# Kernel optimization log

Hardware: AMD Instinct MI355X
Metric: run time of the kernel (lower is better)

Reference implementation:

```python
import jax, jax.numpy as jnp
import numpy as np

BN_EPS = 1e-5

def setup_inputs() -> dict:
    key = jax.random.key(0)
    k1, k2, k3 = jax.random.split(key, 3)
    B, C, H, W = 8, 96, 56, 56
    Cout = 2 * C  # must equal 2*C for the BatchNorm in the original module
    x = jax.random.normal(k1, (B, C, H, W), dtype=jnp.float32)
    conv_w = jax.random.normal(k2, (Cout, 2 * C), dtype=jnp.float32) * (1.0 / np.sqrt(2 * C))
    conv_b = jax.random.normal(k3, (Cout,), dtype=jnp.float32) * 0.01
    gamma = jnp.ones((Cout,), dtype=jnp.float32)
    beta = jnp.zeros((Cout,), dtype=jnp.float32)
    return {"x": x, "conv_w": conv_w, "conv_b": conv_b, "gamma": gamma, "beta": beta}

def _forward(x, conv_w, conv_b, gamma, beta):
    B, C, H, W = x.shape
    # b c h w -> b n c, n = H*W
    q = x.reshape(B, C, H * W).transpose(0, 2, 1)
    # unscaled self-attention (q == k == v == tokens)
    att = jnp.einsum('bnc,bmc->bnm', q, q)          # [B, N, N]
    att = jax.nn.softmax(att, axis=-1)
    att = jnp.einsum('bnm,bmc->bnc', att, q)        # [B, N, C]
    att = att.transpose(0, 2, 1).reshape(B, C, H, W)
    # max-relative: x_j = max(0, x - att) since x_j starts at zeros
    x_j = jnp.maximum(x - att, 0.0)
    cat = jnp.concatenate([x, x_j], axis=1)          # [B, 2C, H, W]
    # 1x1 conv
    y = jnp.einsum('bchw,oc->bohw', cat, conv_w) + conv_b[None, :, None, None]
    # BatchNorm2d in training mode: biased batch stats over (B, H, W)
    mean = jnp.mean(y, axis=(0, 2, 3), keepdims=True)
    var = jnp.var(y, axis=(0, 2, 3), keepdims=True)
    y = (y - mean) * jax.lax.rsqrt(var + BN_EPS)
    y = y * gamma[None, :, None, None] + beta[None, :, None, None]
    # torch nn.GELU default is exact (erf) GELU
    return jax.nn.gelu(y, approximate=False)

def reference(x, conv_w, conv_b, gamma, beta):
    return _forward(x, conv_w, conv_b, gamma, beta)
```

## Files before the change

### kernel.cpp

```cpp
#include <hip/hip_runtime.h>
#include <hip/hip_bf16.h>

#define B_    8
#define C_    96
#define N_    3136
#define COUT_ 192
#define NTOK_ 25088
#define BN_EPS 1e-5f

#define CROW 200
#define BNC  (B_ * N_ * C_)
#define NSPLIT 4
#define NT98  98

#define K2_KL_OFF 7168
#define K2_V_OFF  14336
#define K2_BUFSZ  22528

typedef __hip_bfloat16 bf16;
typedef unsigned short u16;
typedef unsigned int u32;
typedef __attribute__((ext_vector_type(8))) short short8;
typedef __attribute__((ext_vector_type(16))) float f32x16;

__device__ __forceinline__ u16 f2bf(float f) {
    union { __hip_bfloat16 h; u16 u; } cv;
    cv.h = __float2bfloat16(f);
    return cv.u;
}
__device__ __forceinline__ float bf2f(u16 v) {
    union { u16 u; __hip_bfloat16 h; } cv;
    cv.u = v;
    return __bfloat162float(cv.h);
}
__device__ __forceinline__ u32 packbf2(float lo, float hi) {
    return ((u32)f2bf(hi) << 16) | (u32)f2bf(lo);
}

__device__ __forceinline__ void gload_lds16(const void* g, void* l) {
    __builtin_amdgcn_global_load_lds((const __attribute__((address_space(1))) void*)g,
                                     (__attribute__((address_space(3))) void*)l,
                                     16, 0, 0);
}

__global__ __launch_bounds__(256) void transpose_split(const float* __restrict__ x,
                                                       u16* __restrict__ xt_hi,
                                                       u16* __restrict__ xt_lo,
                                                       u16* __restrict__ xc_hi,
                                                       float* __restrict__ norm2) {
    __shared__ float tile[32][33];
    __shared__ float nrm[32];
    const int nb = blockIdx.x * 32;
    const int cb = blockIdx.y * 32;
    const int b  = blockIdx.z;
    const int tid = threadIdx.x;
    const int tx = tid & 31;
    const int ty = tid >> 5;
    if (tid < 32) nrm[tid] = 0.0f;
    float psum = 0.0f;
#pragma unroll
    for (int r = 0; r < 32; r += 8) {
        size_t idx = ((size_t)b * C_ + cb + ty + r) * N_ + nb + tx;
        float v = x[idx];
        tile[ty + r][tx] = v;
        xc_hi[idx] = f2bf(v);
        psum = fmaf(v, v, psum);
    }
    __syncthreads();
    atomicAdd(&nrm[tx], psum);
#pragma unroll
    for (int it = 0; it < 2; it++) {
        const int n2 = (tid >> 4) + it * 16;
        const int cp = tid & 15;
        float v0 = tile[2 * cp][n2];
        float v1 = tile[2 * cp + 1][n2];
        u16 h0 = f2bf(v0), h1 = f2bf(v1);
        u16 l0 = f2bf(v0 - bf2f(h0)), l1 = f2bf(v1 - bf2f(h1));
        size_t o = ((size_t)b * N_ + nb + n2) * C_ + cb + 2 * cp;
        *(u32*)&xt_hi[o] = (u32)h0 | ((u32)h1 << 16);
        *(u32*)&xt_lo[o] = (u32)l0 | ((u32)l1 << 16);
    }
    __syncthreads();
    if (tid < 32)
        atomicAdd(&norm2[(size_t)b * N_ + nb + tid], nrm[tid]);
}

__global__ __launch_bounds__(256) void cast_w(const float* __restrict__ w,
                                              u16* __restrict__ whi,
                                              u16* __restrict__ wlo) {
    int i = blockIdx.x * 256 + threadIdx.x;
    if (i >= COUT_ * 2 * C_) return;
    float v = w[i];
    u16 h = f2bf(v);
    whi[i] = h;
    wlo[i] = f2bf(v - bf2f(h));
}

__global__ __launch_bounds__(256) void norm_max(const float* __restrict__ norm2,
                                                int* __restrict__ maxbits) {
    const int tid = blockIdx.x * 256 + threadIdx.x;
    float m = 0.0f;
    for (int i = tid; i < NTOK_; i += gridDim.x * 256) m = fmaxf(m, norm2[i]);
#pragma unroll
    for (int d = 1; d < 64; d <<= 1) m = fmaxf(m, __shfl_xor(m, d));
    if ((threadIdx.x & 63) == 0) atomicMax(maxbits, __float_as_int(m));
}

__global__ __launch_bounds__(256, 3) void flash_attn_mfma32(const u16* __restrict__ xt_hi,
                                                            const u16* __restrict__ xt_lo,
                                                            const u16* __restrict__ xc_hi,
                                                            const float* __restrict__ norm2,
                                                            const int* __restrict__ maxbits,
                                                            float* __restrict__ attT,
                                                            float* __restrict__ l_arr) {
    __shared__ __align__(16) char LDSU[2][K2_BUFSZ];
    const int b     = blockIdx.y;
    const int i0    = blockIdx.x * 128;
    const int split = blockIdx.z;
    const int kt0   = (NT98 * split) / NSPLIT;
    const int kt1   = (NT98 * (split + 1)) / NSPLIT;
    const int tid   = threadIdx.x;
    const int lane  = tid & 63;
    const int w     = tid >> 6;
    const int col   = lane & 31;
    const int g     = lane >> 5;

    const u16* th = xt_hi + (size_t)b * N_ * C_;
    const u16* tl = xt_lo + (size_t)b * N_ * C_;
    const u16* vh = xc_hi + (size_t)b * C_ * N_;

    u32 loff[6], dofs[6];
#pragma unroll
    for (int j = 0; j < 6; j++) {
        int s = w + 4 * j;
        if (s >= 22) { loff[j] = 0; dofs[j] = 0; continue; }
        if (s < 14) {
            int kind = s < 7 ? 0 : 1;
            int t = s - kind * 7;
            int p = t * 64 + lane;
            int r = p / 13, c = p % 13;
            if (c > 11) c = 11;
            loff[j] = (r < 32) ? (u32)(r * 192 + c * 16) : 0u;
            dofs[j] = (u32)(kind * K2_KL_OFF + t * 1024);
        } else {
            int t = s - 14;
            int p = t * 64 + lane;
            int ch = p / 5, c = p % 5;
            if (c > 3) c = 3;
            loff[j] = (ch < 96) ? (u32)(ch * (N_ * 2) + c * 16) : 0u;
            dofs[j] = (u32)(K2_V_OFF + t * 1024);
        }
    }

    const int qrow  = i0 + w * 32 + col;
    const int qrowc = qrow < N_ ? qrow : N_ - 1;
    short8 qh[6], ql[6];
#pragma unroll
    for (int kc = 0; kc < 6; kc++) {
        qh[kc] = *(const short8*)&th[(size_t)qrowc * C_ + kc * 16 + g * 8];
        ql[kc] = *(const short8*)&tl[(size_t)qrowc * C_ + kc * 16 + g * 8];
    }
    const float maxn2 = __int_as_float(*maxbits);
    const float m_i   = sqrtf(norm2[(size_t)b * N_ + qrowc] * maxn2);
    float l_acc = 0.0f;
    f32x16 O0 = {0}, O1 = {0}, O2 = {0};

    auto stage = [&](int nbuf, int kt) {
        const u32 ktK = (u32)kt * 6144u;
        const u32 ktV = (u32)kt * 64u;
#pragma unroll
        for (int j = 0; j < 6; j++) {
            int s = w + 4 * j;
            if (s >= 22) break;
            const char* sb = (s < 7)  ? (const char*)th + ktK
                           : (s < 14) ? (const char*)tl + ktK
                                      : (const char*)vh + ktV;
            gload_lds16(sb + loff[j], (char*)&LDSU[nbuf][0] + dofs[j]);
        }
    };

    stage(0, kt0);
    __syncthreads();

    const int g16 = g * 16;
    int buf = 0;
    for (int kt = kt0; kt < kt1; kt++) {
        if (kt + 1 < kt1) stage(buf ^ 1, kt + 1);

        const char* Lb = (const char*)&LDSU[buf][0];

        f32x16 S = {0};
        __builtin_amdgcn_s_setprio(1);
#pragma unroll
        for (int kc = 0; kc < 6; kc++) {
            const int o2 = col * 208 + kc * 32 + g16;
            short8 kh = *(const short8*)(Lb + o2);
            short8 kl = *(const short8*)(Lb + K2_KL_OFF + o2);
            S = __builtin_amdgcn_mfma_f32_32x32x16_bf16(kh, ql[kc], S, 0, 0, 0);
            S = __builtin_amdgcn_mfma_f32_32x32x16_bf16(kl, qh[kc], S, 0, 0, 0);
            S = __builtin_amdgcn_mfma_f32_32x32x16_bf16(kh, qh[kc], S, 0, 0, 0);
        }
        __builtin_amdgcn_s_setprio(0);

        float p[16];
#pragma unroll
        for (int r = 0; r < 16; r++) {
            p[r] = __expf(S[r] - m_i);
            l_acc += p[r];
        }
        u32 w8[8];
#pragma unroll
        for (int q = 0; q < 8; q++) w8[q] = packbf2(p[2 * q], p[2 * q + 1]);

        __builtin_amdgcn_s_setprio(1);
#pragma unroll
        for (int kc = 0; kc < 2; kc++) {
            const int qb = kc * 4;
            u32 a0 = w8[qb + 0], a1 = w8[qb + 1];
            u32 a2 = w8[qb + 2], a3 = w8[qb + 3];
            u32 s0 = __shfl_xor((int)a0, 32), s1 = __shfl_xor((int)a1, 32);
            u32 s2 = __shfl_xor((int)a2, 32), s3 = __shfl_xor((int)a3, 32);
            union { short8 v; u32 u[4]; } Bf;
            Bf.u[0] = g ? s2 : a0;
            Bf.u[1] = g ? s3 : a1;
            Bf.u[2] = g ? a2 : s0;
            Bf.u[3] = g ? a3 : s1;
            const int vo = K2_V_OFF + col * 80 + kc * 32 + g16;
            short8 v0 = *(const short8*)(Lb + vo);
            short8 v1 = *(const short8*)(Lb + vo + 2560);
            short8 v2 = *(const short8*)(Lb + vo + 5120);
            O0 = __builtin_amdgcn_mfma_f32_32x32x16_bf16(v0, Bf.v, O0, 0, 0, 0);
            O1 = __builtin_amdgcn_mfma_f32_32x32x16_bf16(v1, Bf.v, O1, 0, 0, 0);
            O2 = __builtin_amdgcn_mfma_f32_32x32x16_bf16(v2, Bf.v, O2, 0, 0, 0);
        }
        __builtin_amdgcn_s_setprio(0);

        __syncthreads();
        buf ^= 1;
    }

    if (qrow < N_) {
        float* ab = attT + (size_t)b * C_ * N_ + qrow;
#pragma unroll
        for (int r = 0; r < 16; r++) {
            int c = (r & 3) + 8 * (r >> 2) + 4 * g;
            atomicAdd(&ab[(size_t)(c)      * N_], O0[r]);
            atomicAdd(&ab[(size_t)(c + 32) * N_], O1[r]);
            atomicAdd(&ab[(size_t)(c + 64) * N_], O2[r]);
        }
        float l_tot = l_acc + __shfl_xor(l_acc, 32);
        if (g == 0) atomicAdd(&l_arr[(size_t)b * N_ + qrow], l_tot);
    }
}

__global__ __launch_bounds__(128, 3) void conv_mfma(const float* __restrict__ x,
                                                    const float* __restrict__ attT,
                                                    const float* __restrict__ l_arr,
                                                    const u16* __restrict__ whi,
                                                    const u16* __restrict__ wlo,
                                                    const float* __restrict__ convb,
                                                    float* __restrict__ y) {
    __shared__ u16 ch[32 * CROW];
    __shared__ u16 cl[32 * CROW];
    __shared__ float invl[32];
    const int b   = blockIdx.x / (N_ / 32);
    const int n0  = (blockIdx.x % (N_ / 32)) * 32;
    const int tid = threadIdx.x;

    if (tid < 32) invl[tid] = 1.0f / l_arr[(size_t)b * N_ + n0 + tid];
    __syncthreads();

    const float* xb = x    + (size_t)b * C_ * N_ + n0;
    const float* ab = attT + (size_t)b * C_ * N_ + n0;
    for (int e = tid; e < 32 * C_; e += 128) {
        int c = e >> 5, t = e & 31;
        float xv = xb[(size_t)c * N_ + t];
        float au = ab[(size_t)c * N_ + t];
        float xj = fmaxf(xv - au * invl[t], 0.0f);
        u16 h1 = f2bf(xv);
        ch[t * CROW + c] = h1;
        cl[t * CROW + c] = f2bf(xv - bf2f(h1));
        u16 h2 = f2bf(xj);
        ch[t * CROW + C_ + c] = h2;
        cl[t * CROW + C_ + c] = f2bf(xj - bf2f(h2));
    }
    __syncthreads();

    const int lane = tid & 63;
    const int w    = tid >> 6;
    const int col  = lane & 31;
    const int g    = lane >> 5;
    const int m0   = w * 3;

    f32x16 A[3] = {{0}, {0}, {0}};
#pragma unroll
    for (int ks = 0; ks < 12; ks++) {
        const int k0 = ks * 16;
        short8 bh = *(const short8*)&ch[col * CROW + k0 + g * 8];
        short8 bl = *(const short8*)&cl[col * CROW + k0 + g * 8];
#pragma unroll
        for (int mt = 0; mt < 3; mt++) {
            const size_t wo = (size_t)((m0 + mt) * 32 + col) * (2 * C_) + k0 + g * 8;
            short8 ah = *(const short8*)&whi[wo];
            short8 al = *(const short8*)&wlo[wo];
            A[mt] = __builtin_amdgcn_mfma_f32_32x32x16_bf16(ah, bl, A[mt], 0, 0, 0);
            A[mt] = __builtin_amdgcn_mfma_f32_32x32x16_bf16(al, bh, A[mt], 0, 0, 0);
            A[mt] = __builtin_amdgcn_mfma_f32_32x32x16_bf16(ah, bh, A[mt], 0, 0, 0);
        }
    }

    float* yb = y + (size_t)b * COUT_ * N_ + n0 + col;
#pragma unroll
    for (int mt = 0; mt < 3; mt++)
#pragma unroll
        for (int r = 0; r < 16; r++) {
            int o = (m0 + mt) * 32 + (r & 3) + 8 * (r >> 2) + 4 * g;
            yb[(size_t)o * N_] = A[mt][r] + convb[o];
        }
}

__global__ __launch_bounds__(256) void bn_partial(const float* __restrict__ y,
                                                  float* __restrict__ pb) {
    const int o   = blockIdx.x;
    const int b   = blockIdx.y;
    const int tid = threadIdx.x;
    float s = 0.0f, q = 0.0f;
    const float4* p = (const float4*)(y + (size_t)(b * COUT_ + o) * N_);
    for (int i = tid; i < N_ / 4; i += 256) {
        float4 v = p[i];
        s += v.x + v.y + v.z + v.w;
        q += v.x * v.x + v.y * v.y + v.z * v.z + v.w * v.w;
    }
#pragma unroll
    for (int d = 1; d < 64; d <<= 1) {
        s += __shfl_xor(s, d);
        q += __shfl_xor(q, d);
    }
    __shared__ float wss[4], wqq[4];
    if ((tid & 63) == 0) { wss[tid >> 6] = s; wqq[tid >> 6] = q; }
    __syncthreads();
    if (tid == 0) {
        pb[b * COUT_ + o]                = wss[0] + wss[1] + wss[2] + wss[3];
        pb[B_ * COUT_ + b * COUT_ + o]   = wqq[0] + wqq[1] + wqq[2] + wqq[3];
    }
}

__global__ __launch_bounds__(192) void bn_finish(const float* __restrict__ pb,
                                                 const float* __restrict__ gamma,
                                                 const float* __restrict__ beta,
                                                 float* __restrict__ ss) {
    const int o = threadIdx.x;
    float s = 0.0f, q = 0.0f;
#pragma unroll
    for (int b = 0; b < B_; b++) {
        s += pb[b * COUT_ + o];
        q += pb[B_ * COUT_ + b * COUT_ + o];
    }
    const float invn = 1.0f / (float)NTOK_;
    float mean = s * invn;
    float var  = q * invn - mean * mean;
    float sc   = gamma[o] * rsqrtf(var + BN_EPS);
    ss[o]         = sc;
    ss[COUT_ + o] = beta[o] - mean * sc;
}

__global__ __launch_bounds__(256) void bn_gelu_out(const float* __restrict__ y,
                                                   const float* __restrict__ ss,
                                                   float* __restrict__ out) {
    const int total4 = (B_ * COUT_ * N_) / 4;
    int i = blockIdx.x * 256 + threadIdx.x;
    if (i >= total4) return;
    int base = i * 4;
    int o = (base / N_) % COUT_;
    float sc = ss[o], sh = ss[COUT_ + o];
    float4 v = *(const float4*)&y[base];
    float u0 = fmaf(v.x, sc, sh), u1 = fmaf(v.y, sc, sh);
    float u2 = fmaf(v.z, sc, sh), u3 = fmaf(v.w, sc, sh);
    const float k = 0.70710678118654752f;
    float4 g;
    g.x = 0.5f * u0 * (1.0f + erff(u0 * k));
    g.y = 0.5f * u1 * (1.0f + erff(u1 * k));
    g.z = 0.5f * u2 * (1.0f + erff(u2 * k));
    g.w = 0.5f * u3 * (1.0f + erff(u3 * k));
    *(float4*)&out[base] = g;
}

extern "C" void kernel_launch(void* const* d_in, const int* in_sizes, int n_in,
                              void* d_out, int out_size, void* d_ws, size_t ws_size,
                              hipStream_t stream) {
    const float* x     = (const float*)d_in[0];
    const float* w     = (const float*)d_in[1];
    const float* cb    = (const float*)d_in[2];
    const float* gamma = (const float*)d_in[3];
    const float* beta  = (const float*)d_in[4];

    u16* xt_hi = (u16*)d_ws;
    u16* xt_lo = xt_hi + (size_t)BNC;
    u16* xc_hi = xt_lo + (size_t)BNC;
    float* attT  = (float*)(xc_hi + (size_t)BNC);
    u16* whi   = (u16*)(attT + (size_t)BNC);
    u16* wlo   = whi + COUT_ * 2 * C_;
    float* y     = (float*)(wlo + COUT_ * 2 * C_);
    float* ss    = y + (size_t)B_ * COUT_ * N_;
    float* l_arr = ss + 2 * COUT_;
    float* norm2 = l_arr + NTOK_;
    int*   maxb  = (int*)(norm2 + NTOK_);
    float* pb    = attT;

    hipMemsetAsync(l_arr, 0, NTOK_ * sizeof(float), stream);
    hipMemsetAsync(norm2, 0, NTOK_ * sizeof(float), stream);
    hipMemsetAsync(maxb, 0, sizeof(int), stream);
    hipMemsetAsync(attT, 0, (size_t)BNC * sizeof(float), stream);

    transpose_split<<<dim3(N_ / 32, C_ / 32, B_), 256, 0, stream>>>(x, xt_hi, xt_lo, xc_hi, norm2);
    cast_w<<<dim3((COUT_ * 2 * C_ + 255) / 256), 256, 0, stream>>>(w, whi, wlo);
    norm_max<<<dim3(25), 256, 0, stream>>>(norm2, maxb);
    flash_attn_mfma32<<<dim3((N_ + 127) / 128, B_, NSPLIT), 256, 0, stream>>>(
        xt_hi, xt_lo, xc_hi, norm2, maxb, attT, l_arr);
    conv_mfma<<<dim3(B_ * (N_ / 32)), 128, 0, stream>>>(x, attT, l_arr, whi, wlo, cb, y);
    bn_partial<<<dim3(COUT_, B_), 256, 0, stream>>>(y, pb);
    bn_finish<<<dim3(1), 192, 0, stream>>>(pb, gamma, beta, ss);
    bn_gelu_out<<<dim3((B_ * COUT_ * N_ / 4 + 255) / 256), 256, 0, stream>>>(y, ss, (float*)d_out);
}
```

Before: 223.7 us.

## Store tokens in MFMA-fragment layout and load K directly from global

The transpose kernel now writes the bf16 hi/lo token matrices in a pre-swizzled layout where each 32-token by 16-channel MFMA operand is a contiguous 512-element block. The attention kernel then loads K fragments straight from global memory (L2-cached) with one 16-byte load per lane, and no longer stages K through LDS. Only V stays double-buffered in LDS. This cuts LDS traffic and footprint, which may allow higher occupancy, but K reads now carry global/L2 latency inside the inner loop with only light software pipelining.

```diff
diff --git a/kernel.cpp b/kernel.cpp
--- a/kernel.cpp
+++ b/kernel.cpp
@@ -13,10 +13,6 @@
 #define NSPLIT 4
 #define NT98  98
 
-#define K2_KL_OFF 7168
-#define K2_V_OFF  14336
-#define K2_BUFSZ  22528
-
 typedef __hip_bfloat16 bf16;
 typedef unsigned short u16;
 typedef unsigned int u32;
@@ -43,9 +39,13 @@
                                      16, 0, 0);
 }
 
+__device__ __forceinline__ size_t foff(int t, int kc) {
+    return ((size_t)t * 6 + kc) << 9;
+}
+
 __global__ __launch_bounds__(256) void transpose_split(const float* __restrict__ x,
-                                                       u16* __restrict__ xt_hi,
-                                                       u16* __restrict__ xt_lo,
+                                                       u16* __restrict__ xf_hi,
+                                                       u16* __restrict__ xf_lo,
                                                        u16* __restrict__ xc_hi,
                                                        float* __restrict__ norm2) {
     __shared__ float tile[32][33];
@@ -68,17 +68,23 @@
     }
     __syncthreads();
     atomicAdd(&nrm[tx], psum);
-#pragma unroll
-    for (int it = 0; it < 2; it++) {
-        const int n2 = (tid >> 4) + it * 16;
-        const int cp = tid & 15;
-        float v0 = tile[2 * cp][n2];
-        float v1 = tile[2 * cp + 1][n2];
-        u16 h0 = f2bf(v0), h1 = f2bf(v1);
-        u16 l0 = f2bf(v0 - bf2f(h0)), l1 = f2bf(v1 - bf2f(h1));
-        size_t o = ((size_t)b * N_ + nb + n2) * C_ + cb + 2 * cp;
-        *(u32*)&xt_hi[o] = (u32)h0 | ((u32)h1 << 16);
-        *(u32*)&xt_lo[o] = (u32)l0 | ((u32)l1 << 16);
+
+    {
+        const int item  = tid & 127;
+        const int is_lo = tid >> 7;
+        const int kc_i  = item >> 6;
+        const int l     = item & 63;
+        const int kcg   = (cb >> 4) + kc_i;
+        union { u16 a[8]; short8 v8; } o;
+#pragma unroll
+        for (int j = 0; j < 8; j++) {
+            float v = tile[kc_i * 16 + ((l >> 5) * 8) + j][l & 31];
+            u16 h = f2bf(v);
+            o.a[j] = is_lo ? f2bf(v - bf2f(h)) : h;
+        }
+        u16* dst = (is_lo ? xf_lo : xf_hi) +
+                   ((size_t)b * NT98 * 6 << 9) + foff(nb >> 5, kcg) + l * 8;
+        *(short8*)dst = o.v8;
     }
     __syncthreads();
     if (tid < 32)
@@ -106,14 +112,14 @@
     if ((threadIdx.x & 63) == 0) atomicMax(maxbits, __float_as_int(m));
 }
 
-__global__ __launch_bounds__(256, 3) void flash_attn_mfma32(const u16* __restrict__ xt_hi,
-                                                            const u16* __restrict__ xt_lo,
+__global__ __launch_bounds__(256, 3) void flash_attn_mfma32(const u16* __restrict__ xf_hi,
+                                                            const u16* __restrict__ xf_lo,
                                                             const u16* __restrict__ xc_hi,
                                                             const float* __restrict__ norm2,
                                                             const int* __restrict__ maxbits,
                                                             float* __restrict__ attT,
                                                             float* __restrict__ l_arr) {
-    __shared__ __align__(16) char LDSU[2][K2_BUFSZ];
+    __shared__ __align__(16) char VL[2][8192];
     const int b     = blockIdx.y;
     const int i0    = blockIdx.x * 128;
     const int split = blockIdx.z;
@@ -125,82 +131,70 @@
     const int col   = lane & 31;
     const int g     = lane >> 5;
 
-    const u16* th = xt_hi + (size_t)b * N_ * C_;
-    const u16* tl = xt_lo + (size_t)b * N_ * C_;
+    const u16* fh = xf_hi + ((size_t)b * NT98 * 6 << 9);
+    const u16* fl = xf_lo + ((size_t)b * NT98 * 6 << 9);
     const u16* vh = xc_hi + (size_t)b * C_ * N_;
 
-    u32 loff[6], dofs[6];
-#pragma unroll
-    for (int j = 0; j < 6; j++) {
+    u32 vloff[2], vdofs[2];
+#pragma unroll
+    for (int j = 0; j < 2; j++) {
         int s = w + 4 * j;
-        if (s >= 22) { loff[j] = 0; dofs[j] = 0; continue; }
-        if (s < 14) {
-            int kind = s < 7 ? 0 : 1;
-            int t = s - kind * 7;
-            int p = t * 64 + lane;
-            int r = p / 13, c = p % 13;
-            if (c > 11) c = 11;
-            loff[j] = (r < 32) ? (u32)(r * 192 + c * 16) : 0u;
-            dofs[j] = (u32)(kind * K2_KL_OFF + t * 1024);
-        } else {
-            int t = s - 14;
-            int p = t * 64 + lane;
-            int ch = p / 5, c = p % 5;
-            if (c > 3) c = 3;
-            loff[j] = (ch < 96) ? (u32)(ch * (N_ * 2) + c * 16) : 0u;
-            dofs[j] = (u32)(K2_V_OFF + t * 1024);
-        }
-    }
-
+        int p = s * 64 + lane;
+        int ch = p / 5, c = p % 5;
+        if (c > 3) c = 3;
+        vloff[j] = (ch < 96) ? (u32)(ch * (N_ * 2) + c * 16) : 0u;
+        vdofs[j] = (u32)(s * 1024);
+    }
+
+    int qt = blockIdx.x * 4 + w;
+    if (qt > NT98 - 1) qt = NT98 - 1;
     const int qrow  = i0 + w * 32 + col;
     const int qrowc = qrow < N_ ? qrow : N_ - 1;
     short8 qh[6], ql[6];
 #pragma unroll
     for (int kc = 0; kc < 6; kc++) {
-        qh[kc] = *(const short8*)&th[(size_t)qrowc * C_ + kc * 16 + g * 8];
-        ql[kc] = *(const short8*)&tl[(size_t)qrowc * C_ + kc * 16 + g * 8];
+        qh[kc] = *(const short8*)&fh[foff(qt, kc) + lane * 8];
+        ql[kc] = *(const short8*)&fl[foff(qt, kc) + lane * 8];
     }
     const float maxn2 = __int_as_float(*maxbits);
     const float m_i   = sqrtf(norm2[(size_t)b * N_ + qrowc] * maxn2);
     float l_acc = 0.0f;
     f32x16 O0 = {0}, O1 = {0}, O2 = {0};
 
-    auto stage = [&](int nbuf, int kt) {
-        const u32 ktK = (u32)kt * 6144u;
+    auto stageV = [&](int nbuf, int kt) {
         const u32 ktV = (u32)kt * 64u;
 #pragma unroll
-        for (int j = 0; j < 6; j++) {
-            int s = w + 4 * j;
-            if (s >= 22) break;
-            const char* sb = (s < 7)  ? (const char*)th + ktK
-                           : (s < 14) ? (const char*)tl + ktK
-                                      : (const char*)vh + ktV;
-            gload_lds16(sb + loff[j], (char*)&LDSU[nbuf][0] + dofs[j]);
-        }
+        for (int j = 0; j < 2; j++)
+            gload_lds16((const char*)vh + ktV + vloff[j], &VL[nbuf][0] + vdofs[j]);
     };
 
-    stage(0, kt0);
+    stageV(0, kt0);
     __syncthreads();
 
     const int g16 = g * 16;
     int buf = 0;
     for (int kt = kt0; kt < kt1; kt++) {
-        if (kt + 1 < kt1) stage(buf ^ 1, kt + 1);
-
-        const char* Lb = (const char*)&LDSU[buf][0];
+        if (kt + 1 < kt1) stageV(buf ^ 1, kt + 1);
 
         f32x16 S = {0};
-        __builtin_amdgcn_s_setprio(1);
-#pragma unroll
-        for (int kc = 0; kc < 6; kc++) {
-            const int o2 = col * 208 + kc * 32 + g16;
-            short8 kh = *(const short8*)(Lb + o2);
-            short8 kl = *(const short8*)(Lb + K2_KL_OFF + o2);
-            S = __builtin_amdgcn_mfma_f32_32x32x16_bf16(kh, ql[kc], S, 0, 0, 0);
-            S = __builtin_amdgcn_mfma_f32_32x32x16_bf16(kl, qh[kc], S, 0, 0, 0);
-            S = __builtin_amdgcn_mfma_f32_32x32x16_bf16(kh, qh[kc], S, 0, 0, 0);
-        }
-        __builtin_amdgcn_s_setprio(0);
+#pragma unroll
+        for (int hf = 0; hf < 2; hf++) {
+            short8 kh[3], kl[3];
+#pragma unroll
+            for (int j = 0; j < 3; j++) {
+                kh[j] = *(const short8*)&fh[foff(kt, hf * 3 + j) + lane * 8];
+                kl[j] = *(const short8*)&fl[foff(kt, hf * 3 + j) + lane * 8];
+            }
+            __builtin_amdgcn_s_setprio(1);
+#pragma unroll
+            for (int j = 0; j < 3; j++) {
+                const int kc = hf * 3 + j;
+                S = __builtin_amdgcn_mfma_f32_32x32x16_bf16(kh[j], ql[kc], S, 0, 0, 0);
+                S = __builtin_amdgcn_mfma_f32_32x32x16_bf16(kl[j], qh[kc], S, 0, 0, 0);
+                S = __builtin_amdgcn_mfma_f32_32x32x16_bf16(kh[j], qh[kc], S, 0, 0, 0);
+            }
+            __builtin_amdgcn_s_setprio(0);
+        }
 
         float p[16];
 #pragma unroll
@@ -225,10 +219,10 @@
             Bf.u[1] = g ? s3 : a1;
             Bf.u[2] = g ? a2 : s0;
             Bf.u[3] = g ? a3 : s1;
-            const int vo = K2_V_OFF + col * 80 + kc * 32 + g16;
-            short8 v0 = *(const short8*)(Lb + vo);
-            short8 v1 = *(const short8*)(Lb + vo + 2560);
-            short8 v2 = *(const short8*)(Lb + vo + 5120);
+            const int vo = col * 80 + kc * 32 + g16;
+            short8 v0 = *(const short8*)(&VL[buf][0] + vo);
+            short8 v1 = *(const short8*)(&VL[buf][0] + vo + 2560);
+            short8 v2 = *(const short8*)(&VL[buf][0] + vo + 5120);
             O0 = __builtin_amdgcn_mfma_f32_32x32x16_bf16(v0, Bf.v, O0, 0, 0, 0);
             O1 = __builtin_amdgcn_mfma_f32_32x32x16_bf16(v1, Bf.v, O1, 0, 0, 0);
             O2 = __builtin_amdgcn_mfma_f32_32x32x16_bf16(v2, Bf.v, O2, 0, 0, 0);
@@ -394,9 +388,9 @@
     const float* gamma = (const float*)d_in[3];
     const float* beta  = (const float*)d_in[4];
 
-    u16* xt_hi = (u16*)d_ws;
-    u16* xt_lo = xt_hi + (size_t)BNC;
-    u16* xc_hi = xt_lo + (size_t)BNC;
+    u16* xf_hi = (u16*)d_ws;
+    u16* xf_lo = xf_hi + (size_t)BNC;
+    u16* xc_hi = xf_lo + (size_t)BNC;
     float* attT  = (float*)(xc_hi + (size_t)BNC);
     u16* whi   = (u16*)(attT + (size_t)BNC);
     u16* wlo   = whi + COUT_ * 2 * C_;
@@ -412,11 +406,11 @@
     hipMemsetAsync(maxb, 0, sizeof(int), stream);
     hipMemsetAsync(attT, 0, (size_t)BNC * sizeof(float), stream);
 
-    transpose_split<<<dim3(N_ / 32, C_ / 32, B_), 256, 0, stream>>>(x, xt_hi, xt_lo, xc_hi, norm2);
+    transpose_split<<<dim3(N_ / 32, C_ / 32, B_), 256, 0, stream>>>(x, xf_hi, xf_lo, xc_hi, norm2);
     cast_w<<<dim3((COUT_ * 2 * C_ + 255) / 256), 256, 0, stream>>>(w, whi, wlo);
     norm_max<<<dim3(25), 256, 0, stream>>>(norm2, maxb);
     flash_attn_mfma32<<<dim3((N_ + 127) / 128, B_, NSPLIT), 256, 0, stream>>>(
-        xt_hi, xt_lo, xc_hi, norm2, maxb, attT, l_arr);
+        xf_hi, xf_lo, xc_hi, norm2, maxb, attT, l_arr);
     conv_mfma<<<dim3(B_ * (N_ / 32)), 128, 0, stream>>>(x, attT, l_arr, whi, wlo, cb, y);
     bn_partial<<<dim3(COUT_, B_), 256, 0, stream>>>(y, pb);
     bn_finish<<<dim3(1), 192, 0, stream>>>(pb, gamma, beta, ss);
```

Result: slower. 242.4 us (+8.4%).
